# Optimization experiments

Measured on AMD Instinct MI355X. Metric: run time of the kernel, lower is better.

The kernel has to match this reference:

```python
import jax, jax.numpy as jnp
import numpy as np

B, H, W, C = 16, 32, 32, 512
HEADS, DHEAD = 8, 64  # head * channel == C
GROUPS, EPS = 32, 1e-5


def setup_inputs() -> dict:
    key = jax.random.key(0)
    ks = jax.random.split(key, 6)
    return {
        "x": jax.random.normal(ks[0], (B, H, W, C), jnp.float32),
        "gn_gamma": jnp.ones((C,), jnp.float32),
        "gn_beta": jnp.zeros((C,), jnp.float32),
        "wq": jax.random.normal(ks[1], (C, HEADS * DHEAD), jnp.float32) * 0.02,
        "wk": jax.random.normal(ks[2], (C, HEADS * DHEAD), jnp.float32) * 0.02,
        "wv": jax.random.normal(ks[3], (C, HEADS * DHEAD), jnp.float32) * 0.02,
        "conv_w": jax.random.normal(ks[4], (3, 3, HEADS * DHEAD, C), jnp.float32) * 0.02,
        "conv_b": jnp.zeros((C,), jnp.float32),
    }


def _group_norm(x, gamma, beta):
    b, h, w, c = x.shape
    xg = x.reshape(b, h, w, GROUPS, c // GROUPS)
    mean = jnp.mean(xg, axis=(1, 2, 4), keepdims=True)
    var = jnp.var(xg, axis=(1, 2, 4), keepdims=True)
    xn = (xg - mean) * jax.lax.rsqrt(var + EPS)
    return xn.reshape(b, h, w, c) * gamma + beta


def reference(x, gn_gamma, gn_beta, wq, wk, wv, conv_w, conv_b):
    xn = _group_norm(x, gn_gamma, gn_beta)          # [B,H,W,C]
    t = xn.reshape(B, H * W, C)                      # tokens [B,S,C]
    q = (t @ wq).reshape(B, H * W, HEADS, DHEAD)
    k = (t @ wk).reshape(B, H * W, HEADS, DHEAD)
    v = (t @ wv).reshape(B, H * W, HEADS, DHEAD)
    scale = 1.0 / jnp.sqrt(jnp.asarray(DHEAD, q.dtype))
    scores = jnp.einsum("bqhd,bkhd->bhqk", q, k) * scale  # [B,HEADS,S,S]
    weights = jax.nn.softmax(scores, axis=-1)
    out = jnp.einsum("bhqk,bkhd->bqhd", weights, v)       # [B,S,HEADS,DHEAD]
    out = out.reshape(B, H, W, HEADS * DHEAD)
    y = jax.lax.conv_general_dilated(
        out, conv_w, window_strides=(1, 1), padding=((1, 1), (1, 1)),
        dimension_numbers=("NHWC", "HWIO", "NHWC")) + conv_b
    return y + x
```

## Files before the change

### kernel.cpp

```cpp
#include <hip/hip_runtime.h>
#include <hip/hip_bf16.h>

#define Bn 16
#define Cc 512
#define Ss 1024
#define HEADS 8
#define DHEAD 64
#define GROUPS 32
#define CPG 16
#define EPSv 1e-5f
#define Mtok (Bn*Ss)
#define QKVS 1536
#define QKS 1024
#define PROW 34
#define PIMG (PROW*PROW)

typedef __hip_bfloat16 bf16;
typedef __attribute__((ext_vector_type(8))) short short8;
typedef __attribute__((ext_vector_type(4))) float f32x4;

union U4 { uint4 u; bf16 h[8]; };
union B4 { ushort4 u; bf16 h[4]; };

__device__ __forceinline__ void stage16(const bf16* g, bf16* l) {
    __builtin_amdgcn_global_load_lds((const __attribute__((address_space(1))) void*)g,
                                     (__attribute__((address_space(3))) void*)l,
                                     16, 0, 0);
}

__device__ __forceinline__ unsigned int pkbf(float a, float b) {
    union { __hip_bfloat16 h; unsigned short u; } ua, ub;
    ua.h = __float2bfloat16(a); ub.h = __float2bfloat16(b);
    return ((unsigned int)ub.u << 16) | ua.u;
}

__device__ __forceinline__ void swz_decode(int F, int& r, int& c) {
    int line = F >> 3, pos = F & 7;
    int u = pos ^ (line & 7);
    r = (line << 1) | (u >> 2);
    c = u & 3;
}
__device__ __forceinline__ int swz_off(int r, int q) {
    return (r >> 1) * 64 + (((((r & 1) << 2) + q) ^ ((r >> 1) & 7)) << 3);
}

__global__ __launch_bounds__(256) void wtrans(const float* __restrict__ src,
                                              bf16* __restrict__ dst) {
    size_t off = (size_t)blockIdx.y * 262144;
    int t = blockIdx.x * 256 + threadIdx.x;
    int n = t & 511, k8 = (t >> 9) * 8;
    const float* s = src + off + (size_t)k8 * 512 + n;
    U4 o;
#pragma unroll
    for (int j = 0; j < 8; j++) o.h[j] = __float2bfloat16(s[(size_t)j * 512]);
    *(uint4*)(dst + off + (size_t)n * 512 + k8) = o.u;
}

__global__ __launch_bounds__(256) void gn_stats(const float* __restrict__ x,
                                                float* __restrict__ stats) {
    int bg = blockIdx.x;
    int b = bg >> 5, g = bg & 31;
    int tid = threadIdx.x;
    const size_t base = (size_t)b * Ss * Cc + g * CPG;
    float sum = 0.f, sq = 0.f;
    for (int i = tid; i < 4096; i += 256) {
        int s = i >> 2, c4 = (i & 3) * 4;
        float4 t = *(const float4*)(x + base + (size_t)s * Cc + c4);
        sum += t.x + t.y + t.z + t.w;
        sq  += t.x * t.x + t.y * t.y + t.z * t.z + t.w * t.w;
    }
    __shared__ float s1[4], s2[4];
#pragma unroll
    for (int off = 32; off > 0; off >>= 1) {
        sum += __shfl_down(sum, off);
        sq  += __shfl_down(sq,  off);
    }
    if ((tid & 63) == 0) { s1[tid >> 6] = sum; s2[tid >> 6] = sq; }
    __syncthreads();
    if (tid == 0) {
        float S = s1[0] + s1[1] + s1[2] + s1[3];
        float Q = s2[0] + s2[1] + s2[2] + s2[3];
        float mean = S * (1.f / 16384.f);
        float var  = Q * (1.f / 16384.f) - mean * mean;
        stats[bg * 2 + 0] = mean;
        stats[bg * 2 + 1] = rsqrtf(var + EPSv);
    }
}

__global__ __launch_bounds__(256) void gn_apply(const float* __restrict__ x,
                                                const float* __restrict__ stats,
                                                const float* __restrict__ gamma,
                                                const float* __restrict__ beta,
                                                bf16* __restrict__ xn) {
    size_t i = (size_t)blockIdx.x * 256 + threadIdx.x;
    size_t e = i * 4;
    int c0 = (int)(e & (Cc - 1));
    int token = (int)(e >> 9);
    int b = token >> 10;
    int g = c0 >> 4;
    float mean = stats[(b * 32 + g) * 2 + 0];
    float rstd = stats[(b * 32 + g) * 2 + 1];
    float4 t  = *(const float4*)(x + e);
    float4 gm = *(const float4*)(gamma + c0);
    float4 bt = *(const float4*)(beta + c0);
    B4 o;
    o.h[0] = __float2bfloat16((t.x - mean) * rstd * gm.x + bt.x);
    o.h[1] = __float2bfloat16((t.y - mean) * rstd * gm.y + bt.y);
    o.h[2] = __float2bfloat16((t.z - mean) * rstd * gm.z + bt.z);
    o.h[3] = __float2bfloat16((t.w - mean) * rstd * gm.w + bt.w);
    *(ushort4*)(xn + e) = o.u;
}

__global__ __launch_bounds__(256) void zero_pad(bf16* __restrict__ Pad) {
    int idx = blockIdx.x * 256 + threadIdx.x;
    int b = idx / (132 * 64);
    int rem = idx - b * 132 * 64;
    int t = rem >> 6, seg = rem & 63;
    int r, c;
    if (t < 34)      { r = 0;  c = t; }
    else if (t < 68) { r = 33; c = t - 34; }
    else { int u = t - 68; r = 1 + (u >> 1); c = (u & 1) * 33; }
    uint4 z = {0u, 0u, 0u, 0u};
    *(uint4*)(Pad + ((size_t)b * PIMG + r * PROW + c) * Cc + seg * 8) = z;
}

__global__ __launch_bounds__(256) void gemm_qkv(const bf16* __restrict__ A,
                                                const bf16* __restrict__ Wt,
                                                bf16* __restrict__ C,
                                                bf16* __restrict__ vT) {
    __shared__ __align__(16) bf16 As[2][4096];
    __shared__ __align__(16) bf16 Bs[2][4096];
    int tid = threadIdx.x;
    int wave = tid >> 6, lane = tid & 63;
    int l15 = lane & 15, quad = lane >> 4;
    int wm = wave >> 1, wn = wave & 1;
    int m0 = blockIdx.y * 128, n0 = blockIdx.x * 128;
    int lr = lane >> 2, kseg = (lane & 3) * 8;
    int ar0 = wave * 32 + lr;

    const bf16* ga = A  + (size_t)(m0 + ar0) * Cc + kseg;
    const bf16* gb = Wt + (size_t)(n0 + ar0) * Cc + kseg;

    auto stageg = [&](int k0, int p) {
        stage16(ga + k0,                   &As[p][wave * 1024]);
        stage16(ga + k0 + (size_t)16 * Cc, &As[p][wave * 1024 + 512]);
        stage16(gb + k0,                   &Bs[p][wave * 1024]);
        stage16(gb + k0 + (size_t)16 * Cc, &Bs[p][wave * 1024 + 512]);
    };

    f32x4 acc[4][4] = {};
    stageg(0, 0);
    for (int it = 0; it < 16; ++it) {
        int p = it & 1;
        if (it + 1 < 16) {
            stageg((it + 1) * 32, p ^ 1);
            asm volatile("s_waitcnt vmcnt(4)" ::: "memory");
        } else {
            asm volatile("s_waitcnt vmcnt(0)" ::: "memory");
        }
        __builtin_amdgcn_s_barrier();

        short8 af[4], bfv[4];
#pragma unroll
        for (int mt = 0; mt < 4; mt++) af[mt]  = *(const short8*)&As[p][(wm * 64 + mt * 16 + l15) * 32 + quad * 8];
#pragma unroll
        for (int nt = 0; nt < 4; nt++) bfv[nt] = *(const short8*)&Bs[p][(wn * 64 + nt * 16 + l15) * 32 + quad * 8];
        asm volatile("s_waitcnt lgkmcnt(0)" ::: "memory");
        __builtin_amdgcn_sched_barrier(0);
        __builtin_amdgcn_s_barrier();

        __builtin_amdgcn_s_setprio(1);
#pragma unroll
        for (int mt = 0; mt < 4; mt++)
#pragma unroll
            for (int nt = 0; nt < 4; nt++)
                acc[mt][nt] = __builtin_amdgcn_mfma_f32_16x16x32_bf16(af[mt], bfv[nt], acc[mt][nt], 0, 0, 0);
        __builtin_amdgcn_s_setprio(0);
    }

    if (n0 < 1024) {
#pragma unroll
        for (int mt = 0; mt < 4; mt++)
#pragma unroll
            for (int r = 0; r < 4; r++) {
                size_t row = (size_t)(m0 + wm * 64 + mt * 16 + quad * 4 + r) * QKS + n0 + wn * 64 + l15;
#pragma unroll
                for (int nt = 0; nt < 4; nt++)
                    C[row + nt * 16] = __float2bfloat16(acc[mt][nt][r]);
            }
    } else {
        int hh = ((n0 - 1024) >> 6) + wn;
        int bq = m0 >> 10;
        int tok0 = (m0 & 1023) + wm * 64;
#pragma unroll
        for (int nt = 0; nt < 4; nt++) {
            int d = nt * 16 + l15;
            bf16* drow = vT + (size_t)(hh * 64 + d) * 16384 + bq * 1024 + tok0;
#pragma unroll
            for (int mt = 0; mt < 4; mt++) {
                B4 o;
#pragma unroll
                for (int r = 0; r < 4; r++) o.h[r] = __float2bfloat16(acc[mt][nt][r]);
                *(ushort4*)(drow + mt * 16 + quad * 4) = o.u;
            }
        }
    }
}

__global__ __launch_bounds__(256) void attention_mfma(const bf16* __restrict__ QK,
                                                      const bf16* __restrict__ vT,
                                                      bf16* __restrict__ Pad) {
    int blk = blockIdx.x;
    int qt = blk & 7;
    int bh = blk >> 3;
    int h = bh & (HEADS - 1), b = bh >> 3;
    int tid = threadIdx.x;
    int wave = tid >> 6, lane = tid & 63;
    int l15 = lane & 15, quad = lane >> 4;

    __shared__ __align__(16) bf16 KT[2][4096];
    __shared__ __align__(16) bf16 VTs[2][4096];

    const size_t base = (size_t)b * Ss * QKS + h * DHEAD;
    const bf16* kbase = QK + base + 512;

    int q0 = qt * 128 + wave * 32;
    const bf16* qrow = QK + base + (size_t)(q0 + l15) * QKS + quad * 8;
    short8 qfA0 = *(const short8*)(qrow);
    short8 qfA1 = *(const short8*)(qrow + 32);
    short8 qfB0 = *(const short8*)(qrow + 16 * QKS);
    short8 qfB1 = *(const short8*)(qrow + 16 * QKS + 32);

    int r1 = tid >> 3,         f1 = (tid & 7) ^ (r1 & 7);
    int r2 = (tid + 256) >> 3, f2 = ((tid + 256) & 7) ^ (r2 & 7);
    const bf16* gk1 = kbase + (size_t)r1 * QKS + f1 * 8;
    const bf16* gk2 = kbase + (size_t)r2 * QKS + f2 * 8;
    const bf16* gv1 = vT + (size_t)(h * 64 + r1) * 16384 + b * 1024 + f1 * 8;
    const bf16* gv2 = vT + (size_t)(h * 64 + r2) * 16384 + b * 1024 + f2 * 8;

    f32x4 oacc0[4] = {{0.f,0.f,0.f,0.f},{0.f,0.f,0.f,0.f},{0.f,0.f,0.f,0.f},{0.f,0.f,0.f,0.f}};
    f32x4 oacc1[4] = {{0.f,0.f,0.f,0.f},{0.f,0.f,0.f,0.f},{0.f,0.f,0.f,0.f},{0.f,0.f,0.f,0.f}};
    float lsum0 = 0.f, lsum1 = 0.f;
    const f32x4 zero4 = {0.f, 0.f, 0.f, 0.f};
    int srcA = ((quad & 1) * 2) * 16 + l15;
    int srcB = srcA + 16;
    bool hiq = (quad >= 2);
    int sw = l15 & 7;

    auto stage = [&](int c0, int p) {
        stage16(gk1 + (size_t)c0 * QKS, &KT[p][wave * 512]);
        stage16(gk2 + (size_t)c0 * QKS, &KT[p][2048 + wave * 512]);
        stage16(gv1 + c0,               &VTs[p][wave * 512]);
        stage16(gv2 + c0,               &VTs[p][2048 + wave * 512]);
    };

    stage(0, 0);
    for (int it = 0; it < 16; ++it) {
        int p = it & 1;
        if (it + 1 < 16) {
            stage((it + 1) * 64, p ^ 1);
            asm volatile("s_waitcnt vmcnt(4)" ::: "memory");
        } else {
            asm volatile("s_waitcnt vmcnt(0)" ::: "memory");
        }
        __builtin_amdgcn_s_barrier();
        __builtin_amdgcn_sched_barrier(0);

        unsigned int pk0[4][2], pk1[4][2];
        __builtin_amdgcn_s_setprio(1);
#pragma unroll
        for (int kb = 0; kb < 4; kb++) {
            const bf16* kr = &KT[p][(kb * 16 + l15) * 64];
            short8 kf0 = *(const short8*)(kr + ((quad ^ sw) * 8));
            short8 kf1 = *(const short8*)(kr + (((4 + quad) ^ sw) * 8));
            f32x4 s0 = __builtin_amdgcn_mfma_f32_16x16x32_bf16(kf0, qfA0, zero4, 0, 0, 0);
            s0 = __builtin_amdgcn_mfma_f32_16x16x32_bf16(kf1, qfA1, s0, 0, 0, 0);
            f32x4 s1 = __builtin_amdgcn_mfma_f32_16x16x32_bf16(kf0, qfB0, zero4, 0, 0, 0);
            s1 = __builtin_amdgcn_mfma_f32_16x16x32_bf16(kf1, qfB1, s1, 0, 0, 0);
            float a0 = __expf(s0[0] * 0.125f);
            float a1 = __expf(s0[1] * 0.125f);
            float a2 = __expf(s0[2] * 0.125f);
            float a3 = __expf(s0[3] * 0.125f);
            lsum0 += (a0 + a1) + (a2 + a3);
            pk0[kb][0] = pkbf(a0, a1);
            pk0[kb][1] = pkbf(a2, a3);
            float b0 = __expf(s1[0] * 0.125f);
            float b1 = __expf(s1[1] * 0.125f);
            float b2 = __expf(s1[2] * 0.125f);
            float b3 = __expf(s1[3] * 0.125f);
            lsum1 += (b0 + b1) + (b2 + b3);
            pk1[kb][0] = pkbf(b0, b1);
            pk1[kb][1] = pkbf(b2, b3);
        }
        __builtin_amdgcn_s_setprio(0);

        union { short8 s8; unsigned int u[4]; } PT00, PT01, PT10, PT11;
        {
            unsigned int A0 = __shfl((int)pk0[0][0], srcA), A1 = __shfl((int)pk0[0][1], srcA);
            unsigned int A2 = __shfl((int)pk0[1][0], srcA), A3 = __shfl((int)pk0[1][1], srcA);
            unsigned int B0 = __shfl((int)pk0[0][0], srcB), B1 = __shfl((int)pk0[0][1], srcB);
            unsigned int B2 = __shfl((int)pk0[1][0], srcB), B3 = __shfl((int)pk0[1][1], srcB);
            PT00.u[0] = hiq ? A2 : A0;  PT00.u[1] = hiq ? A3 : A1;
            PT00.u[2] = hiq ? B2 : B0;  PT00.u[3] = hiq ? B3 : B1;
            unsigned int C0 = __shfl((int)pk0[2][0], srcA), C1 = __shfl((int)pk0[2][1], srcA);
            unsigned int C2 = __shfl((int)pk0[3][0], srcA), C3 = __shfl((int)pk0[3][1], srcA);
            unsigned int D0 = __shfl((int)pk0[2][0], srcB), D1 = __shfl((int)pk0[2][1], srcB);
            unsigned int D2 = __shfl((int)pk0[3][0], srcB), D3 = __shfl((int)pk0[3][1], srcB);
            PT01.u[0] = hiq ? C2 : C0;  PT01.u[1] = hiq ? C3 : C1;
            PT01.u[2] = hiq ? D2 : D0;  PT01.u[3] = hiq ? D3 : D1;
        }
        {
            unsigned int A0 = __shfl((int)pk1[0][0], srcA), A1 = __shfl((int)pk1[0][1], srcA);
            unsigned int A2 = __shfl((int)pk1[1][0], srcA), A3 = __shfl((int)pk1[1][1], srcA);
            unsigned int B0 = __shfl((int)pk1[0][0], srcB), B1 = __shfl((int)pk1[0][1], srcB);
            unsigned int B2 = __shfl((int)pk1[1][0], srcB), B3 = __shfl((int)pk1[1][1], srcB);
            PT10.u[0] = hiq ? A2 : A0;  PT10.u[1] = hiq ? A3 : A1;
            PT10.u[2] = hiq ? B2 : B0;  PT10.u[3] = hiq ? B3 : B1;
            unsigned int C0 = __shfl((int)pk1[2][0], srcA), C1 = __shfl((int)pk1[2][1], srcA);
            unsigned int C2 = __shfl((int)pk1[3][0], srcA), C3 = __shfl((int)pk1[3][1], srcA);
            unsigned int D0 = __shfl((int)pk1[2][0], srcB), D1 = __shfl((int)pk1[2][1], srcB);
            unsigned int D2 = __shfl((int)pk1[3][0], srcB), D3 = __shfl((int)pk1[3][1], srcB);
            PT11.u[0] = hiq ? C2 : C0;  PT11.u[1] = hiq ? C3 : C1;
            PT11.u[2] = hiq ? D2 : D0;  PT11.u[3] = hiq ? D3 : D1;
        }

        __builtin_amdgcn_s_setprio(1);
#pragma unroll
        for (int dt = 0; dt < 4; dt++) {
            const bf16* vr = &VTs[p][(dt * 16 + l15) * 64];
            short8 vf0 = *(const short8*)(vr + ((quad ^ sw) * 8));
            short8 vf1 = *(const short8*)(vr + (((4 + quad) ^ sw) * 8));
            oacc0[dt] = __builtin_amdgcn_mfma_f32_16x16x32_bf16(vf0, PT00.s8, oacc0[dt], 0, 0, 0);
            oacc0[dt] = __builtin_amdgcn_mfma_f32_16x16x32_bf16(vf1, PT01.s8, oacc0[dt], 0, 0, 0);
            oacc1[dt] = __builtin_amdgcn_mfma_f32_16x16x32_bf16(vf0, PT10.s8, oacc1[dt], 0, 0, 0);
            oacc1[dt] = __builtin_amdgcn_mfma_f32_16x16x32_bf16(vf1, PT11.s8, oacc1[dt], 0, 0, 0);
        }
        __builtin_amdgcn_s_setprio(0);

        __builtin_amdgcn_sched_barrier(0);
        __builtin_amdgcn_s_barrier();
        __builtin_amdgcn_sched_barrier(0);
    }

    lsum0 += __shfl_xor(lsum0, 16);
    lsum0 += __shfl_xor(lsum0, 32);
    lsum1 += __shfl_xor(lsum1, 16);
    lsum1 += __shfl_xor(lsum1, 32);
    float inv0 = 1.f / lsum0;
    float inv1 = 1.f / lsum1;

    {
        int s = q0 + l15;
        size_t rowoff = ((size_t)(b * PROW + (s >> 5) + 1) * PROW + (s & 31) + 1) * Cc + h * DHEAD;
#pragma unroll
        for (int dt = 0; dt < 4; dt++) {
            B4 o;
#pragma unroll
            for (int r = 0; r < 4; r++) o.h[r] = __float2bfloat16(oacc0[dt][r] * inv0);
            *(ushort4*)(Pad + rowoff + dt * 16 + quad * 4) = o.u;
        }
    }
    {
        int s = q0 + 16 + l15;
        size_t rowoff = ((size_t)(b * PROW + (s >> 5) + 1) * PROW + (s & 31) + 1) * Cc + h * DHEAD;
#pragma unroll
        for (int dt = 0; dt < 4; dt++) {
            B4 o;
#pragma unroll
            for (int r = 0; r < 4; r++) o.h[r] = __float2bfloat16(oacc1[dt][r] * inv1);
            *(ushort4*)(Pad + rowoff + dt * 16 + quad * 4) = o.u;
        }
    }
}

__global__ __launch_bounds__(256, 2) void conv_mfma(const bf16* __restrict__ Pad,
                                                    const bf16* __restrict__ Wct,
                                                    const float* __restrict__ bias,
                                                    const float* __restrict__ xres,
                                                    float* __restrict__ out) {
    __shared__ __align__(16) bf16 As[2][136 * 32];
    __shared__ __align__(16) bf16 Bs[2][3 * 4096];

    int tid = threadIdx.x;
    int wave = tid >> 6, lane = tid & 63;
    int l15 = lane & 15, quad = lane >> 4;
    int wm = wave >> 1, wn = wave & 1;
    int m0 = blockIdx.y * 128, n0 = blockIdx.x * 128;
    int b = m0 >> 10, oh0 = (m0 & 1023) >> 5;

    int rA1, cA1, rA2, cA2, rA3, cA3;
    swz_decode(tid,              rA1, cA1);
    swz_decode(tid + 256,        rA2, cA2);
    swz_decode((tid & 31) + 512, rA3, cA3);
    int rr1 = rA1 / 34, co1 = rA1 - rr1 * 34;
    int rr2 = rA2 / 34, co2 = rA2 - rr2 * 34;
    int rr3 = rA3 / 34, co3 = rA3 - rr3 * 34;
    const size_t dyStride = (size_t)PROW * Cc;
    const bf16* pA1 = Pad + ((size_t)b * PIMG + (size_t)(oh0 + rr1) * PROW + co1) * Cc + cA1 * 8;
    const bf16* pA2 = Pad + ((size_t)b * PIMG + (size_t)(oh0 + rr2) * PROW + co2) * Cc + cA2 * 8;
    const bf16* pA3 = Pad + ((size_t)b * PIMG + (size_t)(oh0 + rr3) * PROW + co3) * Cc + cA3 * 8;

    int rB1, cB1, rB2, cB2;
    swz_decode(wave * 128 + lane,      rB1, cB1);
    swz_decode(wave * 128 + 64 + lane, rB2, cB2);
    const bf16* gw1 = Wct + (size_t)(n0 + rB1) * Cc + cB1 * 8;
    const bf16* gw2 = Wct + (size_t)(n0 + rB2) * Cc + cB2 * 8;

    int aoff[3][4], boff[4];
#pragma unroll
    for (int mt = 0; mt < 4; mt++) {
        int rbase = (wm * 2 + (mt >> 1)) * 34 + (mt & 1) * 16 + l15;
#pragma unroll
        for (int dxi = 0; dxi < 3; dxi++) aoff[dxi][mt] = swz_off(rbase + dxi, quad);
    }
#pragma unroll
    for (int nt = 0; nt < 4; nt++) boff[nt] = swz_off(wn * 64 + nt * 16 + l15, quad);

    auto stage_it = [&](int it, int p) {
        int dyi = it >> 4;
        int k0 = (it & 15) << 5;
        size_t ag = (size_t)dyi * dyStride + k0;
        stage16(pA1 + ag, &As[p][wave * 512]);
        stage16(pA2 + ag, &As[p][2048 + wave * 512]);
        if (tid < 32) stage16(pA3 + ag, &As[p][4096]);
        size_t wg = (size_t)(dyi * 3) * (Cc * Cc) + k0;
#pragma unroll
        for (int t = 0; t < 3; t++) {
            size_t tg = wg + (size_t)t * (Cc * Cc);
            stage16(gw1 + tg, &Bs[p][t * 4096 + wave * 1024]);
            stage16(gw2 + tg, &Bs[p][t * 4096 + wave * 1024 + 512]);
        }
    };

    f32x4 acc[4][4] = {};
    stage_it(0, 0);
    for (int it = 0; it < 48; ++it) {
        int p = it & 1;
        if (it + 1 < 48) {
            stage_it(it + 1, p ^ 1);
            asm volatile("s_waitcnt vmcnt(8)" ::: "memory");
        } else {
            asm volatile("s_waitcnt vmcnt(0)" ::: "memory");
        }
        __builtin_amdgcn_s_barrier();
        __builtin_amdgcn_sched_barrier(0);

        short8 af[3][4], bfv[3][4];
#pragma unroll
        for (int dxi = 0; dxi < 2; dxi++) {
#pragma unroll
            for (int mt = 0; mt < 4; mt++)
                af[dxi][mt] = *(const short8*)&As[p][aoff[dxi][mt]];
#pragma unroll
            for (int nt = 0; nt < 4; nt++)
                bfv[dxi][nt] = *(const short8*)&Bs[p][dxi * 4096 + boff[nt]];
        }
        __builtin_amdgcn_sched_barrier(0);
        __builtin_amdgcn_s_setprio(1);
#pragma unroll
        for (int mt = 0; mt < 4; mt++)
#pragma unroll
            for (int nt = 0; nt < 4; nt++)
                acc[mt][nt] = __builtin_amdgcn_mfma_f32_16x16x32_bf16(af[0][mt], bfv[0][nt], acc[mt][nt], 0, 0, 0);
        __builtin_amdgcn_s_setprio(0);
        __builtin_amdgcn_sched_barrier(0);
#pragma unroll
        for (int mt = 0; mt < 4; mt++)
            af[2][mt] = *(const short8*)&As[p][aoff[2][mt]];
#pragma unroll
        for (int nt = 0; nt < 4; nt++)
            bfv[2][nt] = *(const short8*)&Bs[p][2 * 4096 + boff[nt]];
        __builtin_amdgcn_sched_barrier(0);
        __builtin_amdgcn_s_setprio(1);
#pragma unroll
        for (int mt = 0; mt < 4; mt++)
#pragma unroll
            for (int nt = 0; nt < 4; nt++)
                acc[mt][nt] = __builtin_amdgcn_mfma_f32_16x16x32_bf16(af[1][mt], bfv[1][nt], acc[mt][nt], 0, 0, 0);
        __builtin_amdgcn_s_setprio(0);
        __builtin_amdgcn_sched_barrier(0);
        asm volatile("s_waitcnt lgkmcnt(0)" ::: "memory");
        __builtin_amdgcn_sched_barrier(0);
        __builtin_amdgcn_s_barrier();
        __builtin_amdgcn_s_setprio(1);
#pragma unroll
        for (int mt = 0; mt < 4; mt++)
#pragma unroll
            for (int nt = 0; nt < 4; nt++)
                acc[mt][nt] = __builtin_amdgcn_mfma_f32_16x16x32_bf16(af[2][mt], bfv[2][nt], acc[mt][nt], 0, 0, 0);
        __builtin_amdgcn_s_setprio(0);
    }

#pragma unroll
    for (int mt = 0; mt < 4; mt++)
#pragma unroll
        for (int r = 0; r < 4; r++) {
            size_t row = (size_t)(m0 + wm * 64 + mt * 16 + quad * 4 + r) * Cc + n0 + wn * 64 + l15;
#pragma unroll
            for (int nt = 0; nt < 4; nt++) {
                int n = n0 + wn * 64 + nt * 16 + l15;
                out[row + nt * 16] = acc[mt][nt][r] + bias[n] + xres[row + nt * 16];
            }
        }
}

extern "C" void kernel_launch(void* const* d_in, const int* in_sizes, int n_in,
                              void* d_out, int out_size, void* d_ws, size_t ws_size,
                              hipStream_t stream) {
    const float* x     = (const float*)d_in[0];
    const float* gamma = (const float*)d_in[1];
    const float* beta  = (const float*)d_in[2];
    const float* wq    = (const float*)d_in[3];
    const float* wk    = (const float*)d_in[4];
    const float* wv    = (const float*)d_in[5];
    const float* convw = (const float*)d_in[6];
    const float* convb = (const float*)d_in[7];
    float* out = (float*)d_out;

    char* ws = (char*)d_ws;
    bf16*  pad   = (bf16*)ws;
    float* stats = (float*)ws;
    bf16*  xn    = (bf16*)(ws + 4096);
    bf16*  wt    = (bf16*)(ws + 4096 + ((size_t)16 << 20));
    bf16*  qk    = (bf16*)(ws + ((size_t)19 << 20));
    bf16*  vt    = (bf16*)(ws + ((size_t)51 << 20));
    bf16*  wct   = (bf16*)(ws + ((size_t)67 << 20));

    wtrans<<<dim3(128, 1), 256, 0, stream>>>(wq, wt);
    wtrans<<<dim3(128, 1), 256, 0, stream>>>(wk, wt + 262144);
    wtrans<<<dim3(128, 1), 256, 0, stream>>>(wv, wt + 524288);
    wtrans<<<dim3(128, 9), 256, 0, stream>>>(convw, wct);

    gn_stats<<<dim3(Bn * GROUPS), 256, 0, stream>>>(x, stats);
    gn_apply<<<dim3(Mtok * Cc / (4 * 256)), 256, 0, stream>>>(x, stats, gamma, beta, xn);

    gemm_qkv<<<dim3(QKVS / 128, Mtok / 128), 256, 0, stream>>>(xn, wt, qk, vt);

    zero_pad<<<dim3(528), 256, 0, stream>>>(pad);
    attention_mfma<<<dim3(Bn * HEADS * (Ss / 128)), 256, 0, stream>>>(qk, vt, pad);

    conv_mfma<<<dim3(Cc / 128, Mtok / 128), 256, 0, stream>>>(pad, wct, convb, x, out);
}
```

Before: 314.3 us.

## Swizzle QKV GEMM LDS layout, merge weight transposes, reorder conv LDS loads

```diff
diff --git a/kernel.cpp b/kernel.cpp
--- a/kernel.cpp
+++ b/kernel.cpp
@@ -42,6 +42,21 @@
 }
 __device__ __forceinline__ int swz_off(int r, int q) {
     return (r >> 1) * 64 + (((((r & 1) << 2) + q) ^ ((r >> 1) & 7)) << 3);
+}
+
+__global__ __launch_bounds__(256) void wtrans3(const float* __restrict__ wq,
+                                               const float* __restrict__ wk,
+                                               const float* __restrict__ wv,
+                                               bf16* __restrict__ dst) {
+    const float* src = (blockIdx.y == 0) ? wq : (blockIdx.y == 1) ? wk : wv;
+    size_t off = (size_t)blockIdx.y * 262144;
+    int t = blockIdx.x * 256 + threadIdx.x;
+    int n = t & 511, k8 = (t >> 9) * 8;
+    const float* s = src + (size_t)k8 * 512 + n;
+    U4 o;
+#pragma unroll
+    for (int j = 0; j < 8; j++) o.h[j] = __float2bfloat16(s[(size_t)j * 512]);
+    *(uint4*)(dst + off + (size_t)n * 512 + k8) = o.u;
 }
 
 __global__ __launch_bounds__(256) void wtrans(const float* __restrict__ src,
@@ -135,17 +150,26 @@
     int l15 = lane & 15, quad = lane >> 4;
     int wm = wave >> 1, wn = wave & 1;
     int m0 = blockIdx.y * 128, n0 = blockIdx.x * 128;
-    int lr = lane >> 2, kseg = (lane & 3) * 8;
-    int ar0 = wave * 32 + lr;
-
-    const bf16* ga = A  + (size_t)(m0 + ar0) * Cc + kseg;
-    const bf16* gb = Wt + (size_t)(n0 + ar0) * Cc + kseg;
+
+    int r0_, c0_, r1_, c1_;
+    swz_decode(wave * 128 + lane,      r0_, c0_);
+    swz_decode(wave * 128 + 64 + lane, r1_, c1_);
+    const bf16* gaS0 = A  + (size_t)(m0 + r0_) * Cc + c0_ * 8;
+    const bf16* gaS1 = A  + (size_t)(m0 + r1_) * Cc + c1_ * 8;
+    const bf16* gbS0 = Wt + (size_t)(n0 + r0_) * Cc + c0_ * 8;
+    const bf16* gbS1 = Wt + (size_t)(n0 + r1_) * Cc + c1_ * 8;
+
+    int aoffg[4], boffg[4];
+#pragma unroll
+    for (int mt = 0; mt < 4; mt++) aoffg[mt] = swz_off(wm * 64 + mt * 16 + l15, quad);
+#pragma unroll
+    for (int nt = 0; nt < 4; nt++) boffg[nt] = swz_off(wn * 64 + nt * 16 + l15, quad);
 
     auto stageg = [&](int k0, int p) {
-        stage16(ga + k0,                   &As[p][wave * 1024]);
-        stage16(ga + k0 + (size_t)16 * Cc, &As[p][wave * 1024 + 512]);
-        stage16(gb + k0,                   &Bs[p][wave * 1024]);
-        stage16(gb + k0 + (size_t)16 * Cc, &Bs[p][wave * 1024 + 512]);
+        stage16(gaS0 + k0, &As[p][wave * 1024]);
+        stage16(gaS1 + k0, &As[p][wave * 1024 + 512]);
+        stage16(gbS0 + k0, &Bs[p][wave * 1024]);
+        stage16(gbS1 + k0, &Bs[p][wave * 1024 + 512]);
     };
 
     f32x4 acc[4][4] = {};
@@ -159,22 +183,28 @@
             asm volatile("s_waitcnt vmcnt(0)" ::: "memory");
         }
         __builtin_amdgcn_s_barrier();
+        __builtin_amdgcn_sched_barrier(0);
 
         short8 af[4], bfv[4];
-#pragma unroll
-        for (int mt = 0; mt < 4; mt++) af[mt]  = *(const short8*)&As[p][(wm * 64 + mt * 16 + l15) * 32 + quad * 8];
-#pragma unroll
-        for (int nt = 0; nt < 4; nt++) bfv[nt] = *(const short8*)&Bs[p][(wn * 64 + nt * 16 + l15) * 32 + quad * 8];
-        asm volatile("s_waitcnt lgkmcnt(0)" ::: "memory");
-        __builtin_amdgcn_sched_barrier(0);
-        __builtin_amdgcn_s_barrier();
+        af[0] = *(const short8*)&As[p][aoffg[0]];
+#pragma unroll
+        for (int nt = 0; nt < 4; nt++) bfv[nt] = *(const short8*)&Bs[p][boffg[nt]];
+#pragma unroll
+        for (int mt = 1; mt < 4; mt++) af[mt] = *(const short8*)&As[p][aoffg[mt]];
 
         __builtin_amdgcn_s_setprio(1);
 #pragma unroll
-        for (int mt = 0; mt < 4; mt++)
+        for (int mt = 0; mt < 3; mt++)
 #pragma unroll
             for (int nt = 0; nt < 4; nt++)
                 acc[mt][nt] = __builtin_amdgcn_mfma_f32_16x16x32_bf16(af[mt], bfv[nt], acc[mt][nt], 0, 0, 0);
+        __builtin_amdgcn_s_setprio(0);
+        asm volatile("s_waitcnt lgkmcnt(0)" ::: "memory");
+        __builtin_amdgcn_s_barrier();
+        __builtin_amdgcn_s_setprio(1);
+#pragma unroll
+        for (int nt = 0; nt < 4; nt++)
+            acc[3][nt] = __builtin_amdgcn_mfma_f32_16x16x32_bf16(af[3], bfv[nt], acc[3][nt], 0, 0, 0);
         __builtin_amdgcn_s_setprio(0);
     }
 
@@ -447,7 +477,7 @@
 
         short8 af[3][4], bfv[3][4];
 #pragma unroll
-        for (int dxi = 0; dxi < 2; dxi++) {
+        for (int dxi = 0; dxi < 3; dxi++) {
 #pragma unroll
             for (int mt = 0; mt < 4; mt++)
                 af[dxi][mt] = *(const short8*)&As[p][aoff[dxi][mt]];
@@ -455,33 +485,20 @@
             for (int nt = 0; nt < 4; nt++)
                 bfv[dxi][nt] = *(const short8*)&Bs[p][dxi * 4096 + boff[nt]];
         }
-        __builtin_amdgcn_sched_barrier(0);
+
         __builtin_amdgcn_s_setprio(1);
 #pragma unroll
-        for (int mt = 0; mt < 4; mt++)
-#pragma unroll
-            for (int nt = 0; nt < 4; nt++)
-                acc[mt][nt] = __builtin_amdgcn_mfma_f32_16x16x32_bf16(af[0][mt], bfv[0][nt], acc[mt][nt], 0, 0, 0);
+        for (int dxi = 0; dxi < 2; dxi++)
+#pragma unroll
+            for (int mt = 0; mt < 4; mt++)
+#pragma unroll
+                for (int nt = 0; nt < 4; nt++)
+                    acc[mt][nt] = __builtin_amdgcn_mfma_f32_16x16x32_bf16(af[dxi][mt], bfv[dxi][nt], acc[mt][nt], 0, 0, 0);
         __builtin_amdgcn_s_setprio(0);
-        __builtin_amdgcn_sched_barrier(0);
-#pragma unroll
-        for (int mt = 0; mt < 4; mt++)
-            af[2][mt] = *(const short8*)&As[p][aoff[2][mt]];
-#pragma unroll
-        for (int nt = 0; nt < 4; nt++)
-            bfv[2][nt] = *(const short8*)&Bs[p][2 * 4096 + boff[nt]];
-        __builtin_amdgcn_sched_barrier(0);
-        __builtin_amdgcn_s_setprio(1);
-#pragma unroll
-        for (int mt = 0; mt < 4; mt++)
-#pragma unroll
-            for (int nt = 0; nt < 4; nt++)
-                acc[mt][nt] = __builtin_amdgcn_mfma_f32_16x16x32_bf16(af[1][mt], bfv[1][nt], acc[mt][nt], 0, 0, 0);
-        __builtin_amdgcn_s_setprio(0);
-        __builtin_amdgcn_sched_barrier(0);
+
         asm volatile("s_waitcnt lgkmcnt(0)" ::: "memory");
-        __builtin_amdgcn_sched_barrier(0);
         __builtin_amdgcn_s_barrier();
+
         __builtin_amdgcn_s_setprio(1);
 #pragma unroll
         for (int mt = 0; mt < 4; mt++)
@@ -526,9 +543,7 @@
     bf16*  vt    = (bf16*)(ws + ((size_t)51 << 20));
     bf16*  wct   = (bf16*)(ws + ((size_t)67 << 20));
 
-    wtrans<<<dim3(128, 1), 256, 0, stream>>>(wq, wt);
-    wtrans<<<dim3(128, 1), 256, 0, stream>>>(wk, wt + 262144);
-    wtrans<<<dim3(128, 1), 256, 0, stream>>>(wv, wt + 524288);
+    wtrans3<<<dim3(128, 3), 256, 0, stream>>>(wq, wk, wv, wt);
     wtrans<<<dim3(128, 9), 256, 0, stream>>>(convw, wct);
 
     gn_stats<<<dim3(Bn * GROUPS), 256, 0, stream>>>(x, stats);
```

Result: no change. 311.5 us (-0.9%).
